# Performance work log

Measured on AMD Instinct MI355X. Metric: run time of the kernel, lower is better.

The kernel has to match this reference:

```python
import jax, jax.numpy as jnp
import numpy as np

TEMPERATURE = 0.07
BASE_TEMPERATURE = 0.07
LAMBDA_HARD = 1.0
HMAX = 1.0
EPS = 1e-8
SIGMA = 1.0  # Gaussian RBF kernel bandwidth on label differences


def setup_inputs() -> dict:
    key = jax.random.key(0)
    k1, k2 = jax.random.split(key)
    features = jax.random.normal(k1, (4096, 2, 128), dtype=jnp.float32)
    labels = jax.random.uniform(k2, (4096,), dtype=jnp.float32)
    return {"features": features, "labels": labels}


def reference(features, labels):
    bsz, n_views, dim = features.shape
    # F.normalize(features, dim=-1)
    feats = features / jnp.sqrt(jnp.sum(features * features, axis=-1, keepdims=True) + 1e-12)
    # torch.cat(torch.unbind(features, dim=1), dim=0) -> view-major stacking [N, dim]
    feats = jnp.transpose(feats, (1, 0, 2)).reshape(bsz * n_views, dim)
    lab = jnp.tile(labels.reshape(bsz, 1), (n_views, 1))  # [N, 1]
    N = bsz * n_views

    logits_mask = 1.0 - jnp.eye(N, dtype=feats.dtype)

    # kernel similarity weights w_{i,k} = K(y_i - y_k), Gaussian RBF, clamped to [0,1]
    dy = lab - lab.T                                   # [N, N]
    w = jnp.clip(jnp.exp(-(dy * dy) / (2.0 * SIGMA * SIGMA)), 0.0, 1.0)

    # hardness term (computed as in source; note w_pos = w, so m is unused downstream)
    d_y = jnp.abs(dy)
    d_y = d_y / (jnp.max(d_y) + EPS)
    sim_cos = feats @ feats.T                          # cosine sim (feats normalized)
    d_z = 1.0 - sim_cos
    d_z = d_z / (jnp.max(d_z) + EPS)
    u = jnp.clip(d_z - d_y, -HMAX, HMAX)
    m = 1.0 + LAMBDA_HARD * jax.nn.relu(u)             # dead code in source; DCE'd under jit

    sim = sim_cos / TEMPERATURE                        # [N, N]
    logits = sim - jax.lax.stop_gradient(jnp.max(sim, axis=1, keepdims=True))
    exp_logits = jnp.exp(logits) * logits_mask
    log_denom = jnp.log(jnp.sum(exp_logits, axis=1, keepdims=True) + EPS)
    log_prob = logits - log_denom

    w_pos_sum = jnp.clip(jnp.sum(w, axis=1), EPS, None)
    mean_log_prob_pos = jnp.sum(w * log_prob, axis=1) / w_pos_sum
    loss = -(TEMPERATURE / BASE_TEMPERATURE) * mean_log_prob_pos
    return jnp.mean(loss)
```

## Files before the change

### kernel.cpp

```cpp
#include <hip/hip_runtime.h>
#include <math.h>

#define BSZ 4096
#define NTOT 8192
#define DIM 128
#define NCHUNK 32

typedef __attribute__((ext_vector_type(8))) short short8;
typedef __attribute__((ext_vector_type(4))) float float4v;

constexpr float INV_T = 1.0f / 0.07f;
constexpr float M0    = INV_T;
constexpr float LOG2E = 1.4426950408889634f;
constexpr float K1    = INV_T * LOG2E;
constexpr float C3    = -0.5f * LOG2E;

__device__ __forceinline__ unsigned short f2bf(float x) {
    union { float f; unsigned u; } u; u.f = x;
    return (unsigned short)((u.u + 0x7FFFu + ((u.u >> 16) & 1)) >> 16);
}
__device__ __forceinline__ float bf2f(unsigned short s) {
    union { unsigned u; float f; } u; u.u = ((unsigned)s) << 16;
    return u.f;
}
__device__ __forceinline__ unsigned pack2(float a, float b) {
    return (unsigned)f2bf(a) | ((unsigned)f2bf(b) << 16);
}

__global__ __launch_bounds__(256) void norm_hsum_k(const float* __restrict__ feat,
                                                   const float* __restrict__ labels,
                                                   unsigned short* __restrict__ F,
                                                   float* __restrict__ h_p,
                                                   float* __restrict__ out) {
    __shared__ unsigned short Fs[32 * DIM];
    __shared__ float hloc[2 * 10 * DIM];

    if (blockIdx.x == 0 && threadIdx.x == 0) out[0] = 0.f;
    const int tid = threadIdx.x;
    const int wv = tid >> 6, l = tid & 63;
    const int g = l >> 3, j = l & 7;
    const int r  = wv * 8 + g;
    const int row = blockIdx.x * 32 + r;
    const int b = row & (BSZ - 1), v = row >> 12;
    const float4* src = reinterpret_cast<const float4*>(feat + (size_t)(b * 2 + v) * DIM) + j * 4;
    const float4 x0 = src[0], x1 = src[1], x2 = src[2], x3 = src[3];
    float s = x0.x*x0.x + x0.y*x0.y + x0.z*x0.z + x0.w*x0.w
            + x1.x*x1.x + x1.y*x1.y + x1.z*x1.z + x1.w*x1.w
            + x2.x*x2.x + x2.y*x2.y + x2.z*x2.z + x2.w*x2.w
            + x3.x*x3.x + x3.y*x3.y + x3.z*x3.z + x3.w*x3.w;
    s += __shfl_xor(s, 1); s += __shfl_xor(s, 2); s += __shfl_xor(s, 4);
    const float inv = 1.0f / sqrtf(s + 1e-12f);
    uint4 w0, w1;
    w0.x = pack2(x0.x*inv, x0.y*inv); w0.y = pack2(x0.z*inv, x0.w*inv);
    w0.z = pack2(x1.x*inv, x1.y*inv); w0.w = pack2(x1.z*inv, x1.w*inv);
    w1.x = pack2(x2.x*inv, x2.y*inv); w1.y = pack2(x2.z*inv, x2.w*inv);
    w1.z = pack2(x3.x*inv, x3.y*inv); w1.w = pack2(x3.z*inv, x3.w*inv);
    uint4* dst = reinterpret_cast<uint4*>(F + (size_t)row * DIM);
    dst[j * 2]     = w0;
    dst[j * 2 + 1] = w1;
    uint4* ldst = reinterpret_cast<uint4*>(Fs + r * DIM);
    ldst[j * 2]     = w0;
    ldst[j * 2 + 1] = w1;
    __syncthreads();

    const int d = tid & 127, hh = tid >> 7;
    const int k0 = blockIdx.x * 32 + hh * 16;
    float acc[10];
#pragma unroll
    for (int m = 0; m < 10; ++m) acc[m] = 0.f;
    for (int kk = 0; kk < 16; ++kk) {
        const int k = k0 + kk;
        const float li = labels[k & (BSZ - 1)];
        const float a = __builtin_amdgcn_exp2f(li * li * C3);
        const float f = bf2f(Fs[(hh * 16 + kk) * DIM + d]);
        float pm = a;
#pragma unroll
        for (int m = 0; m < 10; ++m) {
            acc[m] = fmaf(pm, f, acc[m]);
            pm *= li;
        }
    }
#pragma unroll
    for (int m = 0; m < 10; ++m) hloc[hh * (10 * DIM) + m * DIM + d] = acc[m];
    __syncthreads();

    float* hp = h_p + (size_t)blockIdx.x * (10 * DIM);
    for (int i = tid; i < 10 * DIM; i += 256) hp[i] = hloc[i] + hloc[10 * DIM + i];
}

__global__ __launch_bounds__(1024) void hreduce(const float* __restrict__ h_p,
                                                const float* __restrict__ labels,
                                                float* __restrict__ h,
                                                float* __restrict__ svec) {
    const int m = blockIdx.x;
    const int t = threadIdx.x;
    if (m < 10) {
        __shared__ float red[8][DIM];
        const int d = t & 127, bb = t >> 7;
        float s = 0.f;
#pragma unroll 4
        for (int k = 0; k < 32; ++k)
            s += h_p[(size_t)(bb * 32 + k) * (10 * DIM) + m * DIM + d];
        red[bb][d] = s;
        __syncthreads();
        if (bb == 0) {
            float rr = 0.f;
#pragma unroll
            for (int x = 0; x < 8; ++x) rr += red[x][d];
            h[m * DIM + d] = rr;
        }
    } else {
        __shared__ float sred[16][10];
        float part[10];
#pragma unroll
        for (int mm = 0; mm < 10; ++mm) part[mm] = 0.f;
        for (int k = t; k < NTOT; k += 1024) {
            const float li = labels[k & (BSZ - 1)];
            float pm = __builtin_amdgcn_exp2f(li * li * C3);
#pragma unroll
            for (int mm = 0; mm < 10; ++mm) { part[mm] += pm; pm *= li; }
        }
#pragma unroll
        for (int mm = 0; mm < 10; ++mm) {
#pragma unroll
            for (int off = 32; off >= 1; off >>= 1) part[mm] += __shfl_xor(part[mm], off);
        }
        const int wid = t >> 6;
        if ((t & 63) == 0) {
#pragma unroll
            for (int mm = 0; mm < 10; ++mm) sred[wid][mm] = part[mm];
        }
        __syncthreads();
        if (t < 10) {
            float v = 0.f;
#pragma unroll
            for (int x = 0; x < 16; ++x) v += sred[x][t];
            svec[t] = v;
        }
    }
}

__global__ __launch_bounds__(256) void supcon_mfma(
    const unsigned short* __restrict__ F, float* __restrict__ den_p)
{
    __shared__ __align__(16) unsigned short Bs[2][64 * DIM];

    const int tid = threadIdx.x;
    const int wv  = tid >> 6, l = tid & 63;
    const int l15 = l & 15, lh = l >> 4;
    const int rs  = blockIdx.x >> 5;
    const int cs  = blockIdx.x & 31;
    const int row0 = rs * 256 + wv * 64;
    const int c0   = cs * 256;
    const int ks   = wv * 4 + lh;

#define ISSUE_STAGE(sidx, buf)                                                          \
    {                                                                                   \
        _Pragma("unroll")                                                               \
        for (int q = 0; q < 4; ++q) {                                                   \
            const unsigned short* gsrc =                                                \
                F + (size_t)(c0 + (sidx) * 64 + q * 16 + l15) * DIM + ks * 8;           \
            unsigned short* ldst = &Bs[buf][(q * 256 + wv * 64) * 8];                   \
            __builtin_amdgcn_global_load_lds(                                           \
                (const __attribute__((address_space(1))) unsigned int*)gsrc,            \
                (__attribute__((address_space(3))) unsigned int*)ldst, 16, 0, 0);       \
        }                                                                               \
    }

    ISSUE_STAGE(0, 0);

    short8 a[4][4];
#pragma unroll
    for (int set = 0; set < 4; ++set) {
        const unsigned short* rp = F + (size_t)(row0 + set * 16 + l15) * DIM + lh * 8;
#pragma unroll
        for (int kc = 0; kc < 4; ++kc)
            a[set][kc] = *reinterpret_cast<const short8*>(rp + kc * 32);
    }

    float den[16];
#pragma unroll
    for (int p = 0; p < 16; ++p) den[p] = 0.f;

    for (int s = 0; s < 4; ++s) {
        __syncthreads();
        if (s < 3) ISSUE_STAGE(s + 1, (s + 1) & 1);

        const unsigned short* bs = Bs[s & 1];
#pragma unroll
        for (int sb = 0; sb < 4; ++sb) {
            short8 bfr[4];
#pragma unroll
            for (int kc = 0; kc < 4; ++kc)
                bfr[kc] = *reinterpret_cast<const short8*>(
                    bs + sb * 2048 + (kc * 4 + lh) * 128 + l15 * 8);
            const int col0g = c0 + s * 64 + sb * 16;
#pragma unroll
            for (int set = 0; set < 4; ++set) {
                float4v acc = {0.f, 0.f, 0.f, 0.f};
#pragma unroll
                for (int kc = 0; kc < 4; ++kc)
                    acc = __builtin_amdgcn_mfma_f32_16x16x32_bf16(a[set][kc], bfr[kc], acc, 0, 0, 0);
                const bool dtile = (col0g == row0 + set * 16);
#pragma unroll
                for (int r = 0; r < 4; ++r) {
                    float e = __builtin_amdgcn_exp2f(__builtin_fmaf(acc[r], K1, -K1));
                    if (dtile && (l15 == lh * 4 + r)) e = 0.f;
                    den[set * 4 + r] += e;
                }
            }
        }
    }
#undef ISSUE_STAGE

#pragma unroll
    for (int p = 0; p < 16; ++p) {
        den[p] += __shfl_xor(den[p], 1);
        den[p] += __shfl_xor(den[p], 2);
        den[p] += __shfl_xor(den[p], 4);
        den[p] += __shfl_xor(den[p], 8);
    }
    if (l15 == 0) {
#pragma unroll
        for (int set = 0; set < 4; ++set)
#pragma unroll
            for (int r = 0; r < 4; ++r)
                den_p[(size_t)cs * NTOT + row0 + set * 16 + lh * 4 + r] = den[set * 4 + r];
    }
}

__global__ __launch_bounds__(256) void final_k(const float* __restrict__ feat,
    const float* __restrict__ labels, const float* __restrict__ den_p,
    const float* __restrict__ h, const float* __restrict__ svec,
    float* __restrict__ out)
{
    __shared__ float hs[10 * DIM];
    __shared__ float svs[10];
    __shared__ float wsum[4];
    const int tid = threadIdx.x;
    for (int i = tid; i < 10 * DIM; i += 256) hs[i] = h[i];
    if (tid < 10) svs[tid] = svec[tid];
    __syncthreads();

    const int wv = tid >> 6, l = tid & 63;
    const int g = l >> 3, j = l & 7;
    const int row = blockIdx.x * 32 + wv * 8 + g;
    const int b = row & (BSZ - 1), v = row >> 12;
    const float4* src = reinterpret_cast<const float4*>(feat + (size_t)(b * 2 + v) * DIM) + j * 4;
    const float4 x0 = src[0], x1 = src[1], x2 = src[2], x3 = src[3];
    float s = x0.x*x0.x + x0.y*x0.y + x0.z*x0.z + x0.w*x0.w
            + x1.x*x1.x + x1.y*x1.y + x1.z*x1.z + x1.w*x1.w
            + x2.x*x2.x + x2.y*x2.y + x2.z*x2.z + x2.w*x2.w
            + x3.x*x3.x + x3.y*x3.y + x3.z*x3.z + x3.w*x3.w;
    s += __shfl_xor(s, 1); s += __shfl_xor(s, 2); s += __shfl_xor(s, 4);
    const float inv = 1.0f / sqrtf(s + 1e-12f);

    const float li = labels[b];
    const float ai = __builtin_amdgcn_exp2f(li * li * C3);
    const float cf[10] = {1.f, 1.f, 0.5f, 1.f/6.f, 1.f/24.f, 1.f/120.f,
                          1.f/720.f, 1.f/5040.f, 1.f/40320.f, 1.f/362880.f};
    float swc = 0.f, sw = 0.f, pm = ai;
    const float* hb = &hs[j * 16];
#pragma unroll
    for (int m = 0; m < 10; ++m) {
        const float* hm = hb + m * DIM;
        const float d = x0.x*hm[0]  + x0.y*hm[1]  + x0.z*hm[2]  + x0.w*hm[3]
                      + x1.x*hm[4]  + x1.y*hm[5]  + x1.z*hm[6]  + x1.w*hm[7]
                      + x2.x*hm[8]  + x2.y*hm[9]  + x2.z*hm[10] + x2.w*hm[11]
                      + x3.x*hm[12] + x3.y*hm[13] + x3.z*hm[14] + x3.w*hm[15];
        const float cpm = cf[m] * pm;
        swc = fmaf(cpm, d, swc);
        sw  = fmaf(cpm, svs[m], sw);
        pm *= li;
    }
    swc += __shfl_xor(swc, 1); swc += __shfl_xor(swc, 2); swc += __shfl_xor(swc, 4);
    swc *= inv;

    float dpart = 0.f;
#pragma unroll
    for (int c = 0; c < 4; ++c)
        dpart += den_p[(size_t)(j * 4 + c) * NTOT + row];
    dpart += __shfl_xor(dpart, 1); dpart += __shfl_xor(dpart, 2); dpart += __shfl_xor(dpart, 4);

    const float logd = logf(dpart + 1e-8f);
    const float loss = -(INV_T * swc - (M0 + logd) * sw) / fmaxf(sw, 1e-8f);

    float part = loss * 0.125f;
    part += __shfl_xor(part, 1);  part += __shfl_xor(part, 2);  part += __shfl_xor(part, 4);
    part += __shfl_xor(part, 8);  part += __shfl_xor(part, 16); part += __shfl_xor(part, 32);
    if (l == 0) wsum[wv] = part;
    __syncthreads();
    if (tid == 0)
        atomicAdd(out, (wsum[0] + wsum[1] + wsum[2] + wsum[3]) * (1.0f / NTOT));
}

extern "C" void kernel_launch(void* const* d_in, const int* in_sizes, int n_in,
                              void* d_out, int out_size, void* d_ws, size_t ws_size,
                              hipStream_t stream) {
    const float* feat   = (const float*)d_in[0];
    const float* labels = (const float*)d_in[1];

    char* ws = (char*)d_ws;
    unsigned short* F = (unsigned short*)ws;
    float* den_p = (float*)(ws + (size_t)NTOT * DIM * 2);
    float* h_p   = den_p + (size_t)NCHUNK * NTOT;
    float* h     = h_p + 256 * 10 * DIM;
    float* svec  = h + 10 * DIM;
    float* out   = (float*)d_out;

    norm_hsum_k<<<256, 256, 0, stream>>>(feat, labels, F, h_p, out);
    hreduce<<<11, 1024, 0, stream>>>(h_p, labels, h, svec);
    supcon_mfma<<<1024, 256, 0, stream>>>(F, den_p);
    final_k<<<256, 256, 0, stream>>>(feat, labels, den_p, h, svec, out);
}
```

Before: 96.37 us.

## Fold h-reduction into MFMA kernel blocks and transpose den_p to row-major

Drops the separate hreduce launch. The first 11 blocks of the MFMA similarity kernel now do the h and svec reductions before their normal tile work, which removes one kernel launch and its dependency gap. The den_p partials are stored row-major, one row of chunk sums per sample, so the final kernel reads each lane's four partials with a single float4 load instead of four strided loads. In exchange, those 11 blocks do extra serial work (128-deep reduction loops) and may finish late, and the den_p writes become strided across rows.

After: 115.6 us. +19.9%, slower.

```diff
diff --git a/kernel.cpp b/kernel.cpp
--- a/kernel.cpp
+++ b/kernel.cpp
@@ -88,33 +88,31 @@
     for (int i = tid; i < 10 * DIM; i += 256) hp[i] = hloc[i] + hloc[10 * DIM + i];
 }
 
-__global__ __launch_bounds__(1024) void hreduce(const float* __restrict__ h_p,
-                                                const float* __restrict__ labels,
-                                                float* __restrict__ h,
-                                                float* __restrict__ svec) {
-    const int m = blockIdx.x;
-    const int t = threadIdx.x;
-    if (m < 10) {
-        __shared__ float red[8][DIM];
-        const int d = t & 127, bb = t >> 7;
+__global__ __launch_bounds__(256) void supcon_mfma(
+    const unsigned short* __restrict__ F, const float* __restrict__ labels,
+    const float* __restrict__ h_p, float* __restrict__ h, float* __restrict__ svec,
+    float* __restrict__ den_p)
+{
+    __shared__ __align__(16) unsigned short Bs[2][64 * DIM];
+    __shared__ float comb[DIM];
+    __shared__ float ssred[4][10];
+
+    const int tid = threadIdx.x;
+
+    if (blockIdx.x < 10) {
+        const int m = blockIdx.x;
+        const int d = tid & 127, half = tid >> 7;
         float s = 0.f;
-#pragma unroll 4
-        for (int k = 0; k < 32; ++k)
-            s += h_p[(size_t)(bb * 32 + k) * (10 * DIM) + m * DIM + d];
-        red[bb][d] = s;
+        for (int bb = half * 128; bb < half * 128 + 128; ++bb)
+            s += h_p[(size_t)bb * (10 * DIM) + m * DIM + d];
+        if (half) comb[d] = s;
         __syncthreads();
-        if (bb == 0) {
-            float rr = 0.f;
-#pragma unroll
-            for (int x = 0; x < 8; ++x) rr += red[x][d];
-            h[m * DIM + d] = rr;
-        }
-    } else {
-        __shared__ float sred[16][10];
+        if (!half) h[m * DIM + d] = s + comb[d];
+    } else if (blockIdx.x == 10) {
         float part[10];
 #pragma unroll
         for (int mm = 0; mm < 10; ++mm) part[mm] = 0.f;
-        for (int k = t; k < NTOT; k += 1024) {
+        for (int k = tid; k < NTOT; k += 256) {
             const float li = labels[k & (BSZ - 1)];
             float pm = __builtin_amdgcn_exp2f(li * li * C3);
 #pragma unroll
@@ -125,27 +123,15 @@
 #pragma unroll
             for (int off = 32; off >= 1; off >>= 1) part[mm] += __shfl_xor(part[mm], off);
         }
-        const int wid = t >> 6;
-        if ((t & 63) == 0) {
-#pragma unroll
-            for (int mm = 0; mm < 10; ++mm) sred[wid][mm] = part[mm];
+        if ((tid & 63) == 0) {
+#pragma unroll
+            for (int mm = 0; mm < 10; ++mm) ssred[tid >> 6][mm] = part[mm];
         }
         __syncthreads();
-        if (t < 10) {
-            float v = 0.f;
-#pragma unroll
-            for (int x = 0; x < 16; ++x) v += sred[x][t];
-            svec[t] = v;
-        }
-    }
-}
-
-__global__ __launch_bounds__(256) void supcon_mfma(
-    const unsigned short* __restrict__ F, float* __restrict__ den_p)
-{
-    __shared__ __align__(16) unsigned short Bs[2][64 * DIM];
-
-    const int tid = threadIdx.x;
+        if (tid < 10)
+            svec[tid] = ssred[0][tid] + ssred[1][tid] + ssred[2][tid] + ssred[3][tid];
+    }
+
     const int wv  = tid >> 6, l = tid & 63;
     const int l15 = l & 15, lh = l >> 4;
     const int rs  = blockIdx.x >> 5;
@@ -225,7 +211,7 @@
         for (int set = 0; set < 4; ++set)
 #pragma unroll
             for (int r = 0; r < 4; ++r)
-                den_p[(size_t)cs * NTOT + row0 + set * 16 + lh * 4 + r] = den[set * 4 + r];
+                den_p[(size_t)(row0 + set * 16 + lh * 4 + r) * NCHUNK + cs] = den[set * 4 + r];
     }
 }
 
@@ -276,10 +262,8 @@
     swc += __shfl_xor(swc, 1); swc += __shfl_xor(swc, 2); swc += __shfl_xor(swc, 4);
     swc *= inv;
 
-    float dpart = 0.f;
-#pragma unroll
-    for (int c = 0; c < 4; ++c)
-        dpart += den_p[(size_t)(j * 4 + c) * NTOT + row];
+    const float4 dp4 = *reinterpret_cast<const float4*>(&den_p[(size_t)row * NCHUNK + j * 4]);
+    float dpart = dp4.x + dp4.y + dp4.z + dp4.w;
     dpart += __shfl_xor(dpart, 1); dpart += __shfl_xor(dpart, 2); dpart += __shfl_xor(dpart, 4);
 
     const float logd = logf(dpart + 1e-8f);
@@ -303,13 +287,12 @@
     char* ws = (char*)d_ws;
     unsigned short* F = (unsigned short*)ws;
     float* den_p = (float*)(ws + (size_t)NTOT * DIM * 2);
-    float* h_p   = den_p + (size_t)NCHUNK * NTOT;
+    float* h_p   = den_p + (size_t)NTOT * NCHUNK;
     float* h     = h_p + 256 * 10 * DIM;
     float* svec  = h + 10 * DIM;
     float* out   = (float*)d_out;
 
     norm_hsum_k<<<256, 256, 0, stream>>>(feat, labels, F, h_p, out);
-    hreduce<<<11, 1024, 0, stream>>>(h_p, labels, h, svec);
-    supcon_mfma<<<1024, 256, 0, stream>>>(F, den_p);
+    supcon_mfma<<<1024, 256, 0, stream>>>(F, labels, h_p, h, svec, den_p);
     final_k<<<256, 256, 0, stream>>>(feat, labels, den_p, h, svec, out);
 }
```
